# Optimization experiments

Measured on AMD Instinct MI355X. Metric: run time of the kernel, lower is better.

The kernel has to match this reference:

```python
import jax, jax.numpy as jnp
import numpy as np

B, IN, OUT, D = 8192, 1024, 1024, 8


def setup_inputs() -> dict:
    key = jax.random.key(0)
    k1, k2, k3, k4 = jax.random.split(key, 4)
    # kaiming-uniform-ish init for weights, uniform for biases (values don't affect correctness)
    bound = 1.0 / np.sqrt(IN)
    return {
        "input": jax.random.normal(k1, (B, IN), dtype=jnp.float32),
        "w": jax.random.uniform(k2, (B, D), dtype=jnp.float32),
        "weights": jax.random.uniform(k3, (D, OUT, IN), dtype=jnp.float32, minval=-bound, maxval=bound),
        "biases": jax.random.uniform(k4, (D, OUT), dtype=jnp.float32, minval=-bound, maxval=bound),
    }


def reference(input, w, weights, biases):
    # Original math: weight[b] = sum_d w[b,d] * weights[d]  (shape [out,in])
    #                out[b]    = input[b] @ weight[b].T + sum_d w[b,d]*biases[d]
    # Restructured as one big GEMM + cheap dsize reduction:
    # tmp[b,d,o] = sum_i input[b,i] * weights[d,o,i]   (GEMM: [B,in] x [in, d*out])
    tmp = jnp.einsum('bi,doi->bdo', input, weights)
    out = jnp.einsum('bdo,bd->bo', tmp, w) + w @ biases
    return out
```

## Files before the change

kernel.cpp:

```cpp
#include <hip/hip_runtime.h>
#include <stdint.h>

typedef unsigned short u16;
typedef float v4f __attribute__((ext_vector_type(4)));
typedef short v8s __attribute__((ext_vector_type(8)));

#define B_   8192
#define IN_  1024
#define OUT_ 1024
#define D_   8

#define BM 128
#define BN 128
#define BK 64

__device__ __forceinline__ u16 f2bf(float f) {
  uint32_t u = __float_as_uint(f);
  u += 0x7fffu + ((u >> 16) & 1u);
  return (u16)(u >> 16);
}

__device__ __forceinline__ uint32_t cvtpk(float lo, float hi) {
  uint32_t r;
  asm("v_cvt_pk_bf16_f32 %0, %1, %2" : "=v"(r) : "v"(lo), "v"(hi));
  return r;
}

__global__ __launch_bounds__(256) void convert_w(
    const float* __restrict__ weights, u16* __restrict__ wtBf) {
  const int i4 = blockIdx.x * 256 + threadIdx.x;
  float4 v = ((const float4*)weights)[i4];
  ushort4 o;
  o.x = f2bf(v.x); o.y = f2bf(v.y); o.z = f2bf(v.z); o.w = f2bf(v.w);
  ((ushort4*)wtBf)[i4] = o;
}

__device__ __forceinline__ void gload_lds16(const u16* g, u16* l) {
  typedef __attribute__((address_space(1))) void gvoid;
  typedef __attribute__((address_space(3))) void lvoid;
  __builtin_amdgcn_global_load_lds((gvoid*)g, (lvoid*)l, 16, 0, 0);
}

__global__ __launch_bounds__(256, 2) void gemm_fused(
    const float* __restrict__ Ain,
    const u16* __restrict__ Wt,
    const float* __restrict__ w,
    const float* __restrict__ biases,
    float* __restrict__ out) {
  __shared__ __align__(16) u16 As[2][BM * BK];
  __shared__ __align__(16) u16 Bs[2][BN * BK];

  const int id   = blockIdx.x;
  const int xcd  = id & 7;
  const int slot = id >> 3;
  const int by   = xcd + ((slot & 7) << 3);
  const int bx   = slot >> 3;

  const int tid  = threadIdx.x;
  const int wid  = tid >> 6;
  const int lane = tid & 63;
  const int wr   = wid >> 1, wc = wid & 1;
  const int quad = lane >> 4, l16 = lane & 15;
  const int m0   = by * BM;
  const int n0   = bx * BN;

  const int swz  = (lane & 7) ^ ((lane >> 3) & 7);
  const int rowS = wid * 32 + (lane >> 3);
  const float* aBase[4];
  const u16*   bBase[4];
  int cOff[4];
#pragma unroll
  for (int j = 0; j < 4; ++j) {
    const int row = rowS + j * 8;
    aBase[j] = Ain + (size_t)(m0 + row) * IN_ + swz * 8;
    bBase[j] = Wt  + (size_t)(n0 + row) * IN_ + swz * 8;
    cOff[j]  = (wid * 256 + j * 64 + lane) * 8;
  }

  float4 wA[4], wB[4];
#pragma unroll
  for (int j = 0; j < 4; ++j) {
    const float* wp = w + (size_t)(m0 + rowS + j * 8) * D_;
    wA[j] = ((const float4*)wp)[0];
    wB[j] = ((const float4*)wp)[1];
  }

  const int aRow = wr * 64 + l16;
  const int bRow = wc * 64 + l16;
  const int e    = l16 & 7;
  int aC[2];
#pragma unroll
  for (int h = 0; h < 2; ++h) aC[h] = ((quad + 4 * h) ^ e) * 8;

  const v4f vzero = {0.f, 0.f, 0.f, 0.f};
  v4f acc[4][4];
#pragma unroll
  for (int mt = 0; mt < 4; ++mt)
#pragma unroll
    for (int nt = 0; nt < 4; ++nt) acc[mt][nt] = vzero;

  float4 a0[4], a1[4];

#pragma unroll
  for (int j = 0; j < 4; ++j) {
    const float4* ap = (const float4*)aBase[j];
    a0[j] = ap[0]; a1[j] = ap[1];
  }
#pragma unroll
  for (int j = 0; j < 4; ++j) gload_lds16(bBase[j], &Bs[0][cOff[j]]);
#pragma unroll
  for (int j = 0; j < 4; ++j) {
    const float s = wA[j].x;
    uint4 pk;
    pk.x = cvtpk(a0[j].x * s, a0[j].y * s);
    pk.y = cvtpk(a0[j].z * s, a0[j].w * s);
    pk.z = cvtpk(a1[j].x * s, a1[j].y * s);
    pk.w = cvtpk(a1[j].z * s, a1[j].w * s);
    *(uint4*)(&As[0][cOff[j]]) = pk;
  }
  __builtin_amdgcn_s_waitcnt(0);
  __syncthreads();

  for (int it = 0; it < IN_ / BK; ++it) {
#pragma unroll
    for (int dd = 0; dd < D_; ++dd) {
      const int cur = dd & 1;
      const int nxt = cur ^ 1;
      const int sdd = (dd + 1) & 7;
      const bool last = (it == IN_ / BK - 1) && (dd == D_ - 1);

      if (!last) {
        const int sit = (dd == D_ - 1) ? it + 1 : it;
        if (dd == D_ - 1) {
#pragma unroll
          for (int j = 0; j < 4; ++j) {
            const float4* ap = (const float4*)(aBase[j] + sit * BK);
            a0[j] = ap[0]; a1[j] = ap[1];
          }
        }
#pragma unroll
        for (int j = 0; j < 4; ++j)
          gload_lds16(bBase[j] + (size_t)sdd * (OUT_ * IN_) + sit * BK,
                      &Bs[nxt][cOff[j]]);
      }

#pragma unroll
      for (int h = 0; h < 2; ++h) {
        v8s af[4], bf[4];
#pragma unroll
        for (int mt = 0; mt < 4; ++mt)
          af[mt] = *(const v8s*)(&As[cur][(aRow + mt * 16) * BK + aC[h]]);
#pragma unroll
        for (int nt = 0; nt < 4; ++nt)
          bf[nt] = *(const v8s*)(&Bs[cur][(bRow + nt * 16) * BK + aC[h]]);
#pragma unroll
        for (int mt = 0; mt < 4; ++mt)
#pragma unroll
          for (int nt = 0; nt < 4; ++nt)
            acc[mt][nt] = __builtin_amdgcn_mfma_f32_16x16x32_bf16(
                af[mt], bf[nt], acc[mt][nt], 0, 0, 0);
      }

      if (!last) {
#pragma unroll
        for (int j = 0; j < 4; ++j) {
          const float s = (sdd < 4) ? wA[j][sdd] : wB[j][sdd - 4];
          uint4 pk;
          pk.x = cvtpk(a0[j].x * s, a0[j].y * s);
          pk.y = cvtpk(a0[j].z * s, a0[j].w * s);
          pk.z = cvtpk(a1[j].x * s, a1[j].y * s);
          pk.w = cvtpk(a1[j].z * s, a1[j].w * s);
          *(uint4*)(&As[nxt][cOff[j]]) = pk;
        }
      }
      __builtin_amdgcn_s_waitcnt(0);
      __syncthreads();
    }
  }

  float bcol[4][8];
#pragma unroll
  for (int nt = 0; nt < 4; ++nt) {
    const int col = n0 + wc * 64 + nt * 16 + l16;
#pragma unroll
    for (int dd = 0; dd < 8; ++dd) bcol[nt][dd] = biases[dd * OUT_ + col];
  }
#pragma unroll
  for (int mt = 0; mt < 4; ++mt) {
#pragma unroll
    for (int r = 0; r < 4; ++r) {
      const int grow = m0 + wr * 64 + mt * 16 + quad * 4 + r;
      const v4f* wp = (const v4f*)(w + (size_t)grow * D_);
      const v4f wa = wp[0], wb = wp[1];
#pragma unroll
      for (int nt = 0; nt < 4; ++nt) {
        const int col = n0 + wc * 64 + nt * 16 + l16;
        const float bias = wa[0] * bcol[nt][0] + wa[1] * bcol[nt][1] +
                           wa[2] * bcol[nt][2] + wa[3] * bcol[nt][3] +
                           wb[0] * bcol[nt][4] + wb[1] * bcol[nt][5] +
                           wb[2] * bcol[nt][6] + wb[3] * bcol[nt][7];
        out[(size_t)grow * OUT_ + col] = acc[mt][nt][r] + bias;
      }
    }
  }
}

extern "C" void kernel_launch(void* const* d_in, const int* in_sizes, int n_in,
                              void* d_out, int out_size, void* d_ws, size_t ws_size,
                              hipStream_t stream) {
  const float* input   = (const float*)d_in[0];
  const float* w       = (const float*)d_in[1];
  const float* weights = (const float*)d_in[2];
  const float* biases  = (const float*)d_in[3];
  float* out = (float*)d_out;

  u16* wtBf = (u16*)d_ws;

  const int nF4 = (D_ * OUT_ * IN_) / 4;
  convert_w<<<dim3(nF4 / 256), 256, 0, stream>>>(weights, wtBf);
  gemm_fused<<<dim3(512), 256, 0, stream>>>(input, wtBf, w, biases, out);
}
```

Baseline: 233.7 us.

## Triple-buffer B tiles with prefetch distance two and partial waitcnts

Moves the B operand (bf16 weights) from double to triple buffering in LDS, issuing global_load_lds two phases ahead and waiting with vmcnt thresholds instead of draining all loads before each barrier. The A-tile conversion for the next k-step is moved earlier (at dd==6) so the fp32 input load for the next iteration has more time in flight. It also raises wave priority around the MFMA block and replaces the XCD-aware block swizzle with a plain row-major mapping. The aim is to hide global latency behind MFMAs, at the cost of more LDS (fewer resident blocks possible) and fragile hand-counted vmcnt values.

```diff
diff --git a/kernel.cpp b/kernel.cpp
--- a/kernel.cpp
+++ b/kernel.cpp
@@ -48,13 +48,11 @@
     const float* __restrict__ biases,
     float* __restrict__ out) {
   __shared__ __align__(16) u16 As[2][BM * BK];
-  __shared__ __align__(16) u16 Bs[2][BN * BK];
+  __shared__ __align__(16) u16 Bs[3][BN * BK];
 
   const int id   = blockIdx.x;
-  const int xcd  = id & 7;
-  const int slot = id >> 3;
-  const int by   = xcd + ((slot & 7) << 3);
-  const int bx   = slot >> 3;
+  const int bx   = id & 7;
+  const int by   = id >> 3;
 
   const int tid  = threadIdx.x;
   const int wid  = tid >> 6;
@@ -99,6 +97,10 @@
 #pragma unroll
     for (int nt = 0; nt < 4; ++nt) acc[mt][nt] = vzero;
 
+  u16* bC = Bs[0];
+  u16* bN = Bs[1];
+  u16* bS = Bs[2];
+
   float4 a0[4], a1[4];
 
 #pragma unroll
@@ -107,7 +109,10 @@
     a0[j] = ap[0]; a1[j] = ap[1];
   }
 #pragma unroll
-  for (int j = 0; j < 4; ++j) gload_lds16(bBase[j], &Bs[0][cOff[j]]);
+  for (int j = 0; j < 4; ++j) gload_lds16(bBase[j], bC + cOff[j]);
+#pragma unroll
+  for (int j = 0; j < 4; ++j)
+    gload_lds16(bBase[j] + (size_t)(OUT_ * IN_), bN + cOff[j]);
 #pragma unroll
   for (int j = 0; j < 4; ++j) {
     const float s = wA[j].x;
@@ -118,32 +123,46 @@
     pk.w = cvtpk(a1[j].z * s, a1[j].w * s);
     *(uint4*)(&As[0][cOff[j]]) = pk;
   }
-  __builtin_amdgcn_s_waitcnt(0);
-  __syncthreads();
+  asm volatile("s_waitcnt vmcnt(4) lgkmcnt(0)" ::: "memory");
+  __builtin_amdgcn_s_barrier();
 
   for (int it = 0; it < IN_ / BK; ++it) {
 #pragma unroll
     for (int dd = 0; dd < D_; ++dd) {
       const int cur = dd & 1;
       const int nxt = cur ^ 1;
-      const int sdd = (dd + 1) & 7;
-      const bool last = (it == IN_ / BK - 1) && (dd == D_ - 1);
-
-      if (!last) {
-        const int sit = (dd == D_ - 1) ? it + 1 : it;
-        if (dd == D_ - 1) {
+      const bool lastPhase = (it == 15) && (dd == 7);
+
+      if (dd == 6) {
+#pragma unroll
+        for (int j = 0; j < 4; ++j) {
+          const float s = wB[j].w;
+          uint4 pk;
+          pk.x = cvtpk(a0[j].x * s, a0[j].y * s);
+          pk.y = cvtpk(a0[j].z * s, a0[j].w * s);
+          pk.z = cvtpk(a1[j].x * s, a1[j].y * s);
+          pk.w = cvtpk(a1[j].z * s, a1[j].w * s);
+          *(uint4*)(&As[nxt][cOff[j]]) = pk;
+        }
+        if (it < 15) {
 #pragma unroll
           for (int j = 0; j < 4; ++j) {
-            const float4* ap = (const float4*)(aBase[j] + sit * BK);
+            const float4* ap = (const float4*)(aBase[j] + (it + 1) * BK);
             a0[j] = ap[0]; a1[j] = ap[1];
           }
         }
+      }
+
+      if (!((it == 15) && (dd >= 6))) {
+        const int sdd2 = (dd <= 5) ? dd + 2 : dd - 6;
+        const int sit2 = (dd <= 5) ? it : it + 1;
 #pragma unroll
         for (int j = 0; j < 4; ++j)
-          gload_lds16(bBase[j] + (size_t)sdd * (OUT_ * IN_) + sit * BK,
-                      &Bs[nxt][cOff[j]]);
-      }
-
+          gload_lds16(bBase[j] + (size_t)sdd2 * (OUT_ * IN_) + sit2 * BK,
+                      bS + cOff[j]);
+      }
+
+      __builtin_amdgcn_s_setprio(1);
 #pragma unroll
       for (int h = 0; h < 2; ++h) {
         v8s af[4], bf[4];
@@ -152,7 +171,7 @@
           af[mt] = *(const v8s*)(&As[cur][(aRow + mt * 16) * BK + aC[h]]);
 #pragma unroll
         for (int nt = 0; nt < 4; ++nt)
-          bf[nt] = *(const v8s*)(&Bs[cur][(bRow + nt * 16) * BK + aC[h]]);
+          bf[nt] = *(const v8s*)(bC + (bRow + nt * 16) * BK + aC[h]);
 #pragma unroll
         for (int mt = 0; mt < 4; ++mt)
 #pragma unroll
@@ -160,8 +179,10 @@
             acc[mt][nt] = __builtin_amdgcn_mfma_f32_16x16x32_bf16(
                 af[mt], bf[nt], acc[mt][nt], 0, 0, 0);
       }
-
-      if (!last) {
+      __builtin_amdgcn_s_setprio(0);
+
+      if (dd != 6 && !lastPhase) {
+        const int sdd = (dd + 1) & 7;
 #pragma unroll
         for (int j = 0; j < 4; ++j) {
           const float s = (sdd < 4) ? wA[j][sdd] : wB[j][sdd - 4];
@@ -173,8 +194,20 @@
           *(uint4*)(&As[nxt][cOff[j]]) = pk;
         }
       }
-      __builtin_amdgcn_s_waitcnt(0);
-      __syncthreads();
+
+      if (!lastPhase) {
+        if (dd == 6) {
+          if (it < 15)
+            asm volatile("s_waitcnt vmcnt(12) lgkmcnt(0)" ::: "memory");
+          else
+            asm volatile("s_waitcnt vmcnt(0) lgkmcnt(0)" ::: "memory");
+        } else {
+          asm volatile("s_waitcnt vmcnt(4) lgkmcnt(0)" ::: "memory");
+        }
+        __builtin_amdgcn_s_barrier();
+      }
+
+      u16* tmp = bC; bC = bN; bN = bS; bS = tmp;
     }
   }
 
```

Measured after the change: 233.8 us. About the same (+0.1%).
